# Kernel tuning notes

Hardware: AMD Instinct MI355X
Metric: run time of the kernel (lower is better)

## Reference

```python
import jax, jax.numpy as jnp
import numpy as np

N_NODES = 100000
N_EDGES = 1600000
HID = 64
BN_EPS = 1e-5


def _glorot(key, shape):
    fan_in, fan_out = shape[0], shape[1]
    lim = np.sqrt(6.0 / (fan_in + fan_out))
    return jax.random.uniform(key, shape, jnp.float32, -lim, lim)


def setup_inputs() -> dict:
    key = jax.random.key(0)
    ks = jax.random.split(key, 16)
    inp = {
        "x": jax.random.normal(ks[0], (N_NODES, HID), jnp.float32),
        "edge_index": jax.random.randint(ks[1], (2, N_EDGES), 0, N_NODES, jnp.int64),
        "edge_attr": jax.random.normal(ks[2], (N_EDGES,), jnp.float32),
    }
    # per-layer GIN MLP params: Linear(in,hid) -> BN(hid) -> ReLU -> Linear(hid,out)
    for i in range(2):
        inp[f"W1_{i}"] = _glorot(ks[3 + 5 * i], (HID, HID))
        inp[f"b1_{i}"] = jnp.zeros((HID,), jnp.float32)
        inp[f"gamma_{i}"] = jnp.ones((HID,), jnp.float32)
        inp[f"beta_{i}"] = jnp.zeros((HID,), jnp.float32)
        inp[f"W2_{i}"] = _glorot(ks[4 + 5 * i], (HID, HID))
        inp[f"b2_{i}"] = jnp.zeros((HID,), jnp.float32)
    inp["Wjk"] = _glorot(ks[14], (3 * HID, HID))
    inp["bjk"] = jnp.zeros((HID,), jnp.float32)
    return inp


def _gin_conv(x, src, dst, W1, b1, gamma, beta, W2, b2):
    # GIN aggregation: (1 + eps) * x + sum_{j->i} x_j, eps = 0
    agg = jax.ops.segment_sum(x[src], dst, num_segments=N_NODES)  # [N, d]
    h = (x + agg) @ W1 + b1
    # BatchNorm1d over node dimension (training-style batch statistics)
    mean = jnp.mean(h, axis=0)
    var = jnp.var(h, axis=0)
    h = gamma * (h - mean) * jax.lax.rsqrt(var + BN_EPS) + beta
    h = jax.nn.relu(h)
    return h @ W2 + b2


def reference(x, edge_index, edge_attr,
              W1_0, b1_0, gamma_0, beta_0, W2_0, b2_0,
              W1_1, b1_1, gamma_1, beta_1, W2_1, b2_1,
              Wjk, bjk):
    # edge_attr is accepted but ignored (torch_geometric GINConv does not use it)
    src, dst = edge_index[0], edge_index[1]
    xs = [x]
    h = x
    params = [(W1_0, b1_0, gamma_0, beta_0, W2_0, b2_0),
              (W1_1, b1_1, gamma_1, beta_1, W2_1, b2_1)]
    for p in params:
        h = _gin_conv(h, src, dst, *p)
        h = jax.nn.relu(h)  # dropout p=0.0 is identity
        xs.append(h)
    return jnp.concatenate(xs, axis=-1) @ Wjk + bjk
```

## Files before the change

kernel.cpp:

```cpp
#include <hip/hip_runtime.h>

#define N_NODES 100000
#define N_EDGES 1600000
#define HID 64
#define BN_EPS 1e-5f

#define GATHER_BLOCKS 2048

#define ROW_TILES (N_NODES / 16)
#define TPW1 4
#define G1_BLOCKS ((ROW_TILES + 4*TPW1 - 1) / (4*TPW1))
#define TPW2 2
#define G2_BLOCKS ((ROW_TILES + 4*TPW2 - 1) / (4*TPW2))

#define NB 196
#define MS_BLOCKS 512
#define MS_EPB (N_EDGES / MS_BLOCKS)
#define MS_CNT (NB * MS_BLOCKS)
#define GS_CHUNK 512
#define GS_BLOCKS ((MS_CNT + GS_CHUNK - 1) / GS_CHUNK)

typedef __bf16 bf16x8 __attribute__((ext_vector_type(8)));
typedef float  f32x4  __attribute__((ext_vector_type(4)));
typedef unsigned short u16x8 __attribute__((ext_vector_type(8)));

__device__ __forceinline__ float bf2f(unsigned short u) {
    return __uint_as_float(((unsigned)u) << 16);
}
__device__ __forceinline__ unsigned short f2bf_rne(float f) {
    unsigned u = __float_as_uint(f);
    u += 0x7FFFu + ((u >> 16) & 1u);
    return (unsigned short)(u >> 16);
}

__global__ __launch_bounds__(256) void cvt_bf16_kernel(
        const float* __restrict__ in, unsigned short* __restrict__ out) {
    size_t i = ((size_t)blockIdx.x * 256 + threadIdx.x) * 8;
    if (i >= (size_t)N_NODES * HID) return;
    float4 a = *reinterpret_cast<const float4*>(in + i);
    float4 b = *reinterpret_cast<const float4*>(in + i + 4);
    ushort4 w0 = make_ushort4(f2bf_rne(a.x), f2bf_rne(a.y), f2bf_rne(a.z), f2bf_rne(a.w));
    ushort4 w1 = make_ushort4(f2bf_rne(b.x), f2bf_rne(b.y), f2bf_rne(b.z), f2bf_rne(b.w));
    *reinterpret_cast<ushort4*>(out + i) = w0;
    *reinterpret_cast<ushort4*>(out + i + 4) = w1;
}

__global__ __launch_bounds__(256) void wtrans_all_kernel(
        const float* __restrict__ Wjk,
        const float* __restrict__ W1_0, const float* __restrict__ W2_0,
        const float* __restrict__ W1_1, const float* __restrict__ W2_1,
        unsigned short* __restrict__ wjk_t,
        unsigned short* __restrict__ w1t_0, unsigned short* __restrict__ w2t_0,
        unsigned short* __restrict__ w1t_1, unsigned short* __restrict__ w2t_1) {
    int i = blockIdx.x * 256 + threadIdx.x;
    if (i < 12288) {
        int c = i / 192, k = i - c * 192;
        wjk_t[i] = f2bf_rne(Wjk[k * 64 + c]);
    } else if (i < 12288 + 16384) {
        int r = i - 12288;
        int which = r >> 12, rem = r & 4095;
        int c = rem >> 6, k = rem & 63;
        const float* W = (which == 0) ? W1_0 : (which == 1) ? W2_0
                       : (which == 2) ? W1_1 : W2_1;
        unsigned short* Wt = (which == 0) ? w1t_0 : (which == 1) ? w2t_0
                           : (which == 2) ? w1t_1 : w2t_1;
        Wt[rem] = f2bf_rne(W[k * 64 + c]);
    }
}

__global__ __launch_bounds__(256) void msplit_hist_kernel(
        const int* __restrict__ dst, int* __restrict__ cnt) {
    __shared__ int h[NB];
    for (int i = threadIdx.x; i < NB; i += 256) h[i] = 0;
    __syncthreads();
    const int e0 = blockIdx.x * MS_EPB;
    for (int e = e0 + threadIdx.x; e < e0 + MS_EPB; e += 256)
        atomicAdd(&h[dst[e] >> 9], 1);
    __syncthreads();
    for (int i = threadIdx.x; i < NB; i += 256)
        cnt[i * MS_BLOCKS + blockIdx.x] = h[i];
}

__global__ __launch_bounds__(256) void scan_partial_g(
        const int* __restrict__ in, int* __restrict__ out,
        int* __restrict__ bsums, int n) {
    __shared__ int sd[256];
    int t = threadIdx.x;
    int base = blockIdx.x * GS_CHUNK;
    int i0 = base + 2 * t, i1 = i0 + 1;
    int d0 = (i0 < n) ? in[i0] : 0;
    int d1 = (i1 < n) ? in[i1] : 0;
    sd[t] = d0 + d1;
    __syncthreads();
    for (int o = 1; o < 256; o <<= 1) {
        int v = (t >= o) ? sd[t - o] : 0;
        __syncthreads();
        sd[t] += v;
        __syncthreads();
    }
    int excl = sd[t] - (d0 + d1);
    if (i0 < n) out[i0] = excl;
    if (i1 < n) out[i1] = excl + d0;
    if (t == 255) bsums[blockIdx.x] = sd[255];
}

__global__ __launch_bounds__(256) void scan_bsums_kernel(int* __restrict__ bsums, int nb) {
    __shared__ int sd[256];
    int t = threadIdx.x;
    int v = (t < nb) ? bsums[t] : 0;
    sd[t] = v;
    __syncthreads();
    for (int o = 1; o < 256; o <<= 1) {
        int u = (t >= o) ? sd[t - o] : 0;
        __syncthreads();
        sd[t] += u;
        __syncthreads();
    }
    if (t < nb) bsums[t] = sd[t] - v;
}

__global__ __launch_bounds__(256) void scan_addback_g(
        int* __restrict__ out, const int* __restrict__ bsums, int n, int total) {
    int t = threadIdx.x;
    int b = bsums[blockIdx.x];
    int base = blockIdx.x * GS_CHUNK;
    int i0 = base + 2 * t, i1 = i0 + 1;
    if (i0 < n) out[i0] += b;
    if (i1 < n) out[i1] += b;
    if (blockIdx.x == 0 && t == 0) out[n] = total;
}

__global__ __launch_bounds__(256) void msplit_scatter_kernel(
        const int* __restrict__ src, const int* __restrict__ dst,
        const int* __restrict__ psum, int* __restrict__ bucketed) {
    __shared__ int cur[NB];
    for (int i = threadIdx.x; i < NB; i += 256)
        cur[i] = psum[i * MS_BLOCKS + blockIdx.x];
    __syncthreads();
    const int e0 = blockIdx.x * MS_EPB;
    for (int e = e0 + threadIdx.x; e < e0 + MS_EPB; e += 256) {
        int d = dst[e];
        int p = atomicAdd(&cur[d >> 9], 1);
        bucketed[p] = (src[e] << 9) | (d & 511);
    }
}

__global__ __launch_bounds__(256) void bucket_csr_kernel(
        const int* __restrict__ bucketed, const int* __restrict__ psum,
        int* __restrict__ off, int* __restrict__ eidx) {
    const int j = blockIdx.x;
    const int t = threadIdx.x;
    __shared__ int deg[512];
    __shared__ int sd[256];
    __shared__ int base_s, size_s;
    if (t == 0) {
        int b = psum[j * MS_BLOCKS];
        int nxt = (j == NB - 1) ? N_EDGES : psum[(j + 1) * MS_BLOCKS];
        base_s = b; size_s = nxt - b;
    }
    deg[t] = 0; deg[t + 256] = 0;
    __syncthreads();
    const int base = base_s, size = size_s;
    const int nlo = j << 9;
    for (int i = t; i < size; i += 256)
        atomicAdd(&deg[(unsigned)bucketed[base + i] & 511u], 1);
    __syncthreads();
    int d0 = deg[2 * t], d1 = deg[2 * t + 1];
    sd[t] = d0 + d1;
    __syncthreads();
    for (int o = 1; o < 256; o <<= 1) {
        int v = (t >= o) ? sd[t - o] : 0;
        __syncthreads();
        sd[t] += v;
        __syncthreads();
    }
    int excl = sd[t] - (d0 + d1);
    int g0 = nlo + 2 * t, g1 = g0 + 1;
    if (g0 <= N_NODES) off[g0] = base + excl;
    if (g1 <= N_NODES) off[g1] = base + excl + d0;
    __syncthreads();
    deg[2 * t] = excl;
    deg[2 * t + 1] = excl + d0;
    __syncthreads();
    for (int i = t; i < size; i += 256) {
        unsigned e = (unsigned)bucketed[base + i];
        int p = atomicAdd(&deg[e & 511u], 1);
        eidx[base + p] = (int)(e >> 9);
    }
}

__global__ __launch_bounds__(256) void gather_kernel(
        const unsigned short* __restrict__ xb, const int* __restrict__ off,
        const int* __restrict__ eidx, unsigned short* __restrict__ aggb) {
    const int lane = threadIdx.x & 63;
    const int sub  = lane >> 3;
    const int col  = (lane & 7) << 3;
    const int w    = threadIdx.x >> 6;
    const int gw = blockIdx.x * 4 + w;
    const int stride = gridDim.x * 4;
    for (int n = gw; n < N_NODES; n += stride) {
        const int beg = off[n], end = off[n + 1];
        float acc[8];
#pragma unroll
        for (int i = 0; i < 8; ++i) acc[i] = 0.f;
        for (int j = beg + sub; j < end; j += 8) {
            int s = eidx[j];
            bf16x8 r = *reinterpret_cast<const bf16x8*>(xb + (size_t)s * HID + col);
#pragma unroll
            for (int i = 0; i < 8; ++i) acc[i] += (float)r[i];
        }
#pragma unroll
        for (int m = 8; m <= 32; m <<= 1)
#pragma unroll
            for (int i = 0; i < 8; ++i) acc[i] += __shfl_xor(acc[i], m, 64);
        if (sub == 0) {
            bf16x8 s8 = *reinterpret_cast<const bf16x8*>(xb + (size_t)n * HID + col);
            u16x8 o;
#pragma unroll
            for (int i = 0; i < 8; ++i) o[i] = f2bf_rne(acc[i] + (float)s8[i]);
            *reinterpret_cast<u16x8*>(aggb + (size_t)n * HID + col) = o;
        }
    }
}

__global__ __launch_bounds__(256) void gemm1_mfma_kernel(
        const unsigned short* __restrict__ aggb, const unsigned short* __restrict__ W1t,
        const float* __restrict__ bias, unsigned short* __restrict__ hb,
        float* __restrict__ stats_partial) {
    const int lane = threadIdx.x & 63;
    const int l15 = lane & 15, lhi = lane >> 4;
    const int w = threadIdx.x >> 6;

    bf16x8 bfrag[2][4];
    float bs[4];
#pragma unroll
    for (int f = 0; f < 4; ++f) {
        const unsigned short* wp = W1t + (size_t)(f * 16 + l15) * 64 + lhi * 8;
        bfrag[0][f] = *reinterpret_cast<const bf16x8*>(wp);
        bfrag[1][f] = *reinterpret_cast<const bf16x8*>(wp + 32);
        bs[f] = bias[f * 16 + l15];
    }

    float ssum[4] = {0.f, 0.f, 0.f, 0.f}, ssq[4] = {0.f, 0.f, 0.f, 0.f};

    const int tile0 = (blockIdx.x * 4 + w) * TPW1;
#pragma unroll
    for (int tt = 0; tt < TPW1; ++tt) {
        const int tile = tile0 + tt;
        if (tile < ROW_TILES) {
            const int r0 = tile * 16;
            const size_t arow = (size_t)(r0 + l15) * 64 + lhi * 8;
            bf16x8 a0 = *reinterpret_cast<const bf16x8*>(aggb + arow);
            bf16x8 a1 = *reinterpret_cast<const bf16x8*>(aggb + arow + 32);
            f32x4 acc[4];
#pragma unroll
            for (int f = 0; f < 4; ++f) acc[f] = (f32x4){bs[f], bs[f], bs[f], bs[f]};
#pragma unroll
            for (int f = 0; f < 4; ++f) {
                acc[f] = __builtin_amdgcn_mfma_f32_16x16x32_bf16(a0, bfrag[0][f], acc[f], 0, 0, 0);
                acc[f] = __builtin_amdgcn_mfma_f32_16x16x32_bf16(a1, bfrag[1][f], acc[f], 0, 0, 0);
            }
#pragma unroll
            for (int f = 0; f < 4; ++f)
#pragma unroll
                for (int i = 0; i < 4; ++i) {
                    hb[(size_t)(r0 + lhi * 4 + i) * 64 + f * 16 + l15] = f2bf_rne(acc[f][i]);
                    ssum[f] += acc[f][i];
                    ssq[f]  += acc[f][i] * acc[f][i];
                }
        }
    }

    __shared__ float red[2][4][256];
#pragma unroll
    for (int f = 0; f < 4; ++f) {
        red[0][f][threadIdx.x] = ssum[f];
        red[1][f][threadIdx.x] = ssq[f];
    }
    __syncthreads();
    if (threadIdx.x < 64) {
        int c = threadIdx.x, f = c >> 4, p = c & 15;
        float s = 0.f, q = 0.f;
#pragma unroll
        for (int u = 0; u < 16; ++u) {
            int t = (u >> 2) * 64 + (u & 3) * 16 + p;
            s += red[0][f][t];
            q += red[1][f][t];
        }
        stats_partial[(size_t)blockIdx.x * 128 + c]      = s;
        stats_partial[(size_t)blockIdx.x * 128 + 64 + c] = q;
    }
}

__global__ __launch_bounds__(256) void bn_gemm_mfma_kernel(
        const unsigned short* __restrict__ hb, const unsigned short* __restrict__ W2t,
        const float* __restrict__ bias, const float* __restrict__ scale,
        const float* __restrict__ shift, unsigned short* __restrict__ outb) {
    const int lane = threadIdx.x & 63;
    const int l15 = lane & 15, lhi = lane >> 4;
    const int w = threadIdx.x >> 6;

    bf16x8 bfrag[2][4];
    float bs[4];
#pragma unroll
    for (int f = 0; f < 4; ++f) {
        const unsigned short* wp = W2t + (size_t)(f * 16 + l15) * 64 + lhi * 8;
        bfrag[0][f] = *reinterpret_cast<const bf16x8*>(wp);
        bfrag[1][f] = *reinterpret_cast<const bf16x8*>(wp + 32);
        bs[f] = bias[f * 16 + l15];
    }
    float sc[2][8], sh[2][8];
#pragma unroll
    for (int t = 0; t < 2; ++t)
#pragma unroll
        for (int j = 0; j < 8; ++j) {
            int k = t * 32 + lhi * 8 + j;
            sc[t][j] = scale[k];
            sh[t][j] = shift[k];
        }

    const int tile0 = (blockIdx.x * 4 + w) * TPW2;
#pragma unroll
    for (int tt = 0; tt < TPW2; ++tt) {
        const int tile = tile0 + tt;
        if (tile >= ROW_TILES) return;
        const int r0 = tile * 16;
        f32x4 acc[4];
#pragma unroll
        for (int f = 0; f < 4; ++f) acc[f] = (f32x4){bs[f], bs[f], bs[f], bs[f]};
#pragma unroll
        for (int t = 0; t < 2; ++t) {
            const unsigned short* hp = hb + (size_t)(r0 + l15) * 64 + t * 32 + lhi * 8;
            bf16x8 raw = *reinterpret_cast<const bf16x8*>(hp);
            bf16x8 a;
#pragma unroll
            for (int j = 0; j < 8; ++j)
                a[j] = (__bf16)fmaxf(fmaf(sc[t][j], (float)raw[j], sh[t][j]), 0.f);
#pragma unroll
            for (int f = 0; f < 4; ++f)
                acc[f] = __builtin_amdgcn_mfma_f32_16x16x32_bf16(a, bfrag[t][f], acc[f], 0, 0, 0);
        }
#pragma unroll
        for (int f = 0; f < 4; ++f)
#pragma unroll
            for (int i = 0; i < 4; ++i)
                outb[(size_t)(r0 + lhi * 4 + i) * 64 + f * 16 + l15] =
                    f2bf_rne(fmaxf(acc[f][i], 0.f));
    }
}

__global__ __launch_bounds__(256) void jumphead_mfma_kernel(
        const unsigned short* __restrict__ xb, const unsigned short* __restrict__ h1b,
        const unsigned short* __restrict__ h2b, const unsigned short* __restrict__ Wt,
        const float* __restrict__ bjk, float* __restrict__ out) {
    const int lane = threadIdx.x & 63;
    const int l15 = lane & 15, lhi = lane >> 4;
    const int w = threadIdx.x >> 6;

    bf16x8 bfrag[6][4];
    float bs[4];
#pragma unroll
    for (int f = 0; f < 4; ++f) {
        const unsigned short* wp = Wt + (size_t)(f * 16 + l15) * 192 + lhi * 8;
#pragma unroll
        for (int t = 0; t < 6; ++t)
            bfrag[t][f] = *reinterpret_cast<const bf16x8*>(wp + t * 32);
        bs[f] = bjk[f * 16 + l15];
    }

    const int tile0 = (blockIdx.x * 4 + w) * TPW2;
#pragma unroll
    for (int tt = 0; tt < TPW2; ++tt) {
        const int tile = tile0 + tt;
        if (tile >= ROW_TILES) return;
        const int r0 = tile * 16;
        const size_t arow = (size_t)(r0 + l15) * 64 + lhi * 8;
        bf16x8 a0 = *reinterpret_cast<const bf16x8*>(xb + arow);
        bf16x8 a1 = *reinterpret_cast<const bf16x8*>(xb + arow + 32);
        bf16x8 a2 = *reinterpret_cast<const bf16x8*>(h1b + arow);
        bf16x8 a3 = *reinterpret_cast<const bf16x8*>(h1b + arow + 32);
        bf16x8 a4 = *reinterpret_cast<const bf16x8*>(h2b + arow);
        bf16x8 a5 = *reinterpret_cast<const bf16x8*>(h2b + arow + 32);
        f32x4 acc[4];
#pragma unroll
        for (int f = 0; f < 4; ++f) acc[f] = (f32x4){bs[f], bs[f], bs[f], bs[f]};
#pragma unroll
        for (int f = 0; f < 4; ++f) {
            acc[f] = __builtin_amdgcn_mfma_f32_16x16x32_bf16(a0, bfrag[0][f], acc[f], 0, 0, 0);
            acc[f] = __builtin_amdgcn_mfma_f32_16x16x32_bf16(a1, bfrag[1][f], acc[f], 0, 0, 0);
            acc[f] = __builtin_amdgcn_mfma_f32_16x16x32_bf16(a2, bfrag[2][f], acc[f], 0, 0, 0);
            acc[f] = __builtin_amdgcn_mfma_f32_16x16x32_bf16(a3, bfrag[3][f], acc[f], 0, 0, 0);
            acc[f] = __builtin_amdgcn_mfma_f32_16x16x32_bf16(a4, bfrag[4][f], acc[f], 0, 0, 0);
            acc[f] = __builtin_amdgcn_mfma_f32_16x16x32_bf16(a5, bfrag[5][f], acc[f], 0, 0, 0);
        }
#pragma unroll
        for (int f = 0; f < 4; ++f)
#pragma unroll
            for (int i = 0; i < 4; ++i)
                out[(size_t)(r0 + lhi * 4 + i) * 64 + f * 16 + l15] = acc[f][i];
    }
}

__global__ __launch_bounds__(1024) void bn_finalize_kernel(
        const float* __restrict__ stats_partial, int nblocks,
        const float* __restrict__ gamma, const float* __restrict__ beta,
        float* __restrict__ scale, float* __restrict__ shift) {
    __shared__ float red[2][1024];
    const int t = threadIdx.x;
    const int c = t & 63;
    const int chunk = t >> 6;
    float s = 0.f, q = 0.f;
    for (int b = chunk; b < nblocks; b += 16) {
        s += stats_partial[(size_t)b * 128 + c];
        q += stats_partial[(size_t)b * 128 + 64 + c];
    }
    red[0][t] = s;
    red[1][t] = q;
    __syncthreads();
    if (chunk == 0) {
        float ss = 0.f, qq = 0.f;
#pragma unroll
        for (int k = 0; k < 16; ++k) {
            ss += red[0][k * 64 + c];
            qq += red[1][k * 64 + c];
        }
        float mean = ss / (float)N_NODES;
        float var  = qq / (float)N_NODES - mean * mean;
        float scl  = gamma[c] * rsqrtf(var + BN_EPS);
        scale[c] = scl;
        shift[c] = beta[c] - mean * scl;
    }
}

extern "C" void kernel_launch(void* const* d_in, const int* in_sizes, int n_in,
                              void* d_out, int out_size, void* d_ws, size_t ws_size,
                              hipStream_t stream) {
    const float* x    = (const float*)d_in[0];
    const int*   ei   = (const int*)d_in[1];
    const int*   src  = ei;
    const int*   dst  = ei + N_EDGES;
    const float* W1_0 = (const float*)d_in[3];
    const float* b1_0 = (const float*)d_in[4];
    const float* g_0  = (const float*)d_in[5];
    const float* be_0 = (const float*)d_in[6];
    const float* W2_0 = (const float*)d_in[7];
    const float* b2_0 = (const float*)d_in[8];
    const float* W1_1 = (const float*)d_in[9];
    const float* b1_1 = (const float*)d_in[10];
    const float* g_1  = (const float*)d_in[11];
    const float* be_1 = (const float*)d_in[12];
    const float* W2_1 = (const float*)d_in[13];
    const float* b2_1 = (const float*)d_in[14];
    const float* Wjk  = (const float*)d_in[15];
    const float* bjk  = (const float*)d_in[16];

    const size_t FEAT = (size_t)N_NODES * HID;

    unsigned short* aggb = (unsigned short*)d_ws;
    unsigned short* hb   = aggb + FEAT;
    unsigned short* xb   = hb + FEAT;
    unsigned short* h1b  = xb + FEAT;
    unsigned short* h2b  = h1b + FEAT;
    float* stats = (float*)(h2b + FEAT);
    float* scale = stats + (size_t)G1_BLOCKS * 128;
    float* shift = scale + 64;
    int*   off   = (int*)(shift + 64);
    int*   eidx  = off + N_NODES + 2;
    int*   cnt   = eidx + N_EDGES;
    int*   psum  = cnt + MS_CNT;
    int*   bsums = psum + MS_CNT + 2;
    unsigned short* wjk_t = (unsigned short*)(bsums + 256);
    unsigned short* w2t_0 = wjk_t + 64 * 192;
    unsigned short* w2t_1 = w2t_0 + 64 * 64;
    unsigned short* w1t_0 = w2t_1 + 64 * 64;
    unsigned short* w1t_1 = w1t_0 + 64 * 64;
    int*   bucketed = (int*)h2b;
    float* out   = (float*)d_out;

    cvt_bf16_kernel<<<(int)(FEAT / 8 / 256), 256, 0, stream>>>(x, xb);
    wtrans_all_kernel<<<(12288 + 16384 + 255) / 256, 256, 0, stream>>>(
        Wjk, W1_0, W2_0, W1_1, W2_1, wjk_t, w1t_0, w2t_0, w1t_1, w2t_1);

    msplit_hist_kernel<<<MS_BLOCKS, 256, 0, stream>>>(dst, cnt);
    scan_partial_g<<<GS_BLOCKS, 256, 0, stream>>>(cnt, psum, bsums, MS_CNT);
    scan_bsums_kernel<<<1, 256, 0, stream>>>(bsums, GS_BLOCKS);
    scan_addback_g<<<GS_BLOCKS, 256, 0, stream>>>(psum, bsums, MS_CNT, N_EDGES);
    msplit_scatter_kernel<<<MS_BLOCKS, 256, 0, stream>>>(src, dst, psum, bucketed);
    bucket_csr_kernel<<<NB, 256, 0, stream>>>(bucketed, psum, off, eidx);

    gather_kernel<<<GATHER_BLOCKS, 256, 0, stream>>>(xb, off, eidx, aggb);
    gemm1_mfma_kernel<<<G1_BLOCKS, 256, 0, stream>>>(aggb, w1t_0, b1_0, hb, stats);
    bn_finalize_kernel<<<1, 1024, 0, stream>>>(stats, G1_BLOCKS, g_0, be_0, scale, shift);
    bn_gemm_mfma_kernel<<<G2_BLOCKS, 256, 0, stream>>>(hb, w2t_0, b2_0, scale, shift, h1b);

    gather_kernel<<<GATHER_BLOCKS, 256, 0, stream>>>(h1b, off, eidx, aggb);
    gemm1_mfma_kernel<<<G1_BLOCKS, 256, 0, stream>>>(aggb, w1t_1, b1_1, hb, stats);
    bn_finalize_kernel<<<1, 1024, 0, stream>>>(stats, G1_BLOCKS, g_1, be_1, scale, shift);
    bn_gemm_mfma_kernel<<<G2_BLOCKS, 256, 0, stream>>>(hb, w2t_1, b2_1, scale, shift, h2b);

    jumphead_mfma_kernel<<<G2_BLOCKS, 256, 0, stream>>>(
        xb, h1b, h2b, wjk_t, bjk, out);
}
```

Before: 220.0 us.

## Use 8-lane groups per node in gather and finer 256-node CSR buckets

The gather kernel now gives each node an 8-lane group that walks its whole edge list serially, two edges per step. This replaces the old scheme where one wave handled one node, split its edges across 8 sub-groups and reduced them with shuffles, so the shuffle reduction and grid-stride loop are gone and one block covers 32 nodes. The CSR build moves from 512-node to 256-node buckets with more partition blocks, and the block-sums scan is widened to handle up to 1024 entries. Per-node load imbalance now falls on individual lane groups, and there are more histogram/scan entries to process.

```diff
diff --git a/kernel.cpp b/kernel.cpp
--- a/kernel.cpp
+++ b/kernel.cpp
@@ -5,7 +5,7 @@
 #define HID 64
 #define BN_EPS 1e-5f
 
-#define GATHER_BLOCKS 2048
+#define GATHER_BLOCKS (N_NODES / 32)
 
 #define ROW_TILES (N_NODES / 16)
 #define TPW1 4
@@ -13,8 +13,8 @@
 #define TPW2 2
 #define G2_BLOCKS ((ROW_TILES + 4*TPW2 - 1) / (4*TPW2))
 
-#define NB 196
-#define MS_BLOCKS 512
+#define NB 391
+#define MS_BLOCKS 1000
 #define MS_EPB (N_EDGES / MS_BLOCKS)
 #define MS_CNT (NB * MS_BLOCKS)
 #define GS_CHUNK 512
@@ -75,7 +75,7 @@
     __syncthreads();
     const int e0 = blockIdx.x * MS_EPB;
     for (int e = e0 + threadIdx.x; e < e0 + MS_EPB; e += 256)
-        atomicAdd(&h[dst[e] >> 9], 1);
+        atomicAdd(&h[dst[e] >> 8], 1);
     __syncthreads();
     for (int i = threadIdx.x; i < NB; i += 256)
         cnt[i * MS_BLOCKS + blockIdx.x] = h[i];
@@ -107,8 +107,14 @@
 __global__ __launch_bounds__(256) void scan_bsums_kernel(int* __restrict__ bsums, int nb) {
     __shared__ int sd[256];
     int t = threadIdx.x;
-    int v = (t < nb) ? bsums[t] : 0;
-    sd[t] = v;
+    int v[4]; int s = 0;
+#pragma unroll
+    for (int k = 0; k < 4; ++k) {
+        int i = t * 4 + k;
+        v[k] = (i < nb) ? bsums[i] : 0;
+        s += v[k];
+    }
+    sd[t] = s;
     __syncthreads();
     for (int o = 1; o < 256; o <<= 1) {
         int u = (t >= o) ? sd[t - o] : 0;
@@ -116,7 +122,13 @@
         sd[t] += u;
         __syncthreads();
     }
-    if (t < nb) bsums[t] = sd[t] - v;
+    int run = sd[t] - s;
+#pragma unroll
+    for (int k = 0; k < 4; ++k) {
+        int i = t * 4 + k;
+        if (i < nb) bsums[i] = run;
+        run += v[k];
+    }
 }
 
 __global__ __launch_bounds__(256) void scan_addback_g(
@@ -140,8 +152,8 @@
     const int e0 = blockIdx.x * MS_EPB;
     for (int e = e0 + threadIdx.x; e < e0 + MS_EPB; e += 256) {
         int d = dst[e];
-        int p = atomicAdd(&cur[d >> 9], 1);
-        bucketed[p] = (src[e] << 9) | (d & 511);
+        int p = atomicAdd(&cur[d >> 8], 1);
+        bucketed[p] = (src[e] << 8) | (d & 255);
     }
 }
 
@@ -150,7 +162,7 @@
         int* __restrict__ off, int* __restrict__ eidx) {
     const int j = blockIdx.x;
     const int t = threadIdx.x;
-    __shared__ int deg[512];
+    __shared__ int deg[256];
     __shared__ int sd[256];
     __shared__ int base_s, size_s;
     if (t == 0) {
@@ -158,15 +170,15 @@
         int nxt = (j == NB - 1) ? N_EDGES : psum[(j + 1) * MS_BLOCKS];
         base_s = b; size_s = nxt - b;
     }
-    deg[t] = 0; deg[t + 256] = 0;
+    deg[t] = 0;
     __syncthreads();
     const int base = base_s, size = size_s;
-    const int nlo = j << 9;
+    const int nlo = j << 8;
     for (int i = t; i < size; i += 256)
-        atomicAdd(&deg[(unsigned)bucketed[base + i] & 511u], 1);
-    __syncthreads();
-    int d0 = deg[2 * t], d1 = deg[2 * t + 1];
-    sd[t] = d0 + d1;
+        atomicAdd(&deg[(unsigned)bucketed[base + i] & 255u], 1);
+    __syncthreads();
+    int d0 = deg[t];
+    sd[t] = d0;
     __syncthreads();
     for (int o = 1; o < 256; o <<= 1) {
         int v = (t >= o) ? sd[t - o] : 0;
@@ -174,18 +186,16 @@
         sd[t] += v;
         __syncthreads();
     }
-    int excl = sd[t] - (d0 + d1);
-    int g0 = nlo + 2 * t, g1 = g0 + 1;
+    int excl = sd[t] - d0;
+    int g0 = nlo + t;
     if (g0 <= N_NODES) off[g0] = base + excl;
-    if (g1 <= N_NODES) off[g1] = base + excl + d0;
-    __syncthreads();
-    deg[2 * t] = excl;
-    deg[2 * t + 1] = excl + d0;
+    __syncthreads();
+    deg[t] = excl;
     __syncthreads();
     for (int i = t; i < size; i += 256) {
         unsigned e = (unsigned)bucketed[base + i];
-        int p = atomicAdd(&deg[e & 511u], 1);
-        eidx[base + p] = (int)(e >> 9);
+        int p = atomicAdd(&deg[e & 255u], 1);
+        eidx[base + p] = (int)(e >> 8);
     }
 }
 
@@ -193,34 +203,36 @@
         const unsigned short* __restrict__ xb, const int* __restrict__ off,
         const int* __restrict__ eidx, unsigned short* __restrict__ aggb) {
     const int lane = threadIdx.x & 63;
-    const int sub  = lane >> 3;
+    const int g    = lane >> 3;
     const int col  = (lane & 7) << 3;
     const int w    = threadIdx.x >> 6;
-    const int gw = blockIdx.x * 4 + w;
-    const int stride = gridDim.x * 4;
-    for (int n = gw; n < N_NODES; n += stride) {
-        const int beg = off[n], end = off[n + 1];
-        float acc[8];
-#pragma unroll
-        for (int i = 0; i < 8; ++i) acc[i] = 0.f;
-        for (int j = beg + sub; j < end; j += 8) {
-            int s = eidx[j];
-            bf16x8 r = *reinterpret_cast<const bf16x8*>(xb + (size_t)s * HID + col);
-#pragma unroll
-            for (int i = 0; i < 8; ++i) acc[i] += (float)r[i];
-        }
-#pragma unroll
-        for (int m = 8; m <= 32; m <<= 1)
-#pragma unroll
-            for (int i = 0; i < 8; ++i) acc[i] += __shfl_xor(acc[i], m, 64);
-        if (sub == 0) {
-            bf16x8 s8 = *reinterpret_cast<const bf16x8*>(xb + (size_t)n * HID + col);
-            u16x8 o;
-#pragma unroll
-            for (int i = 0; i < 8; ++i) o[i] = f2bf_rne(acc[i] + (float)s8[i]);
-            *reinterpret_cast<u16x8*>(aggb + (size_t)n * HID + col) = o;
-        }
-    }
+    const int n = blockIdx.x * 32 + w * 8 + g;
+
+    const int beg = off[n], end = off[n + 1];
+    bf16x8 s8 = *reinterpret_cast<const bf16x8*>(xb + (size_t)n * HID + col);
+    float acc[8];
+#pragma unroll
+    for (int i = 0; i < 8; ++i) acc[i] = (float)s8[i];
+
+    int j = beg;
+    for (; j + 2 <= end; j += 2) {
+        int s0 = eidx[j], s1 = eidx[j + 1];
+        bf16x8 r0 = *reinterpret_cast<const bf16x8*>(xb + (size_t)s0 * HID + col);
+        bf16x8 r1 = *reinterpret_cast<const bf16x8*>(xb + (size_t)s1 * HID + col);
+#pragma unroll
+        for (int i = 0; i < 8; ++i) acc[i] += (float)r0[i] + (float)r1[i];
+    }
+    if (j < end) {
+        int s0 = eidx[j];
+        bf16x8 r0 = *reinterpret_cast<const bf16x8*>(xb + (size_t)s0 * HID + col);
+#pragma unroll
+        for (int i = 0; i < 8; ++i) acc[i] += (float)r0[i];
+    }
+
+    u16x8 o;
+#pragma unroll
+    for (int i = 0; i < 8; ++i) o[i] = f2bf_rne(acc[i]);
+    *reinterpret_cast<u16x8*>(aggb + (size_t)n * HID + col) = o;
 }
 
 __global__ __launch_bounds__(256) void gemm1_mfma_kernel(
@@ -469,7 +481,7 @@
     int*   cnt   = eidx + N_EDGES;
     int*   psum  = cnt + MS_CNT;
     int*   bsums = psum + MS_CNT + 2;
-    unsigned short* wjk_t = (unsigned short*)(bsums + 256);
+    unsigned short* wjk_t = (unsigned short*)(bsums + 1024);
     unsigned short* w2t_0 = wjk_t + 64 * 192;
     unsigned short* w2t_1 = w2t_0 + 64 * 64;
     unsigned short* w1t_0 = w2t_1 + 64 * 64;
```

Result: faster. 204.0 us (-7.3%).
